# Kernel optimization log

Measured on AMD Instinct MI355X. Metric: run time of the kernel, lower is better.

The kernel has to match this reference:

```python
import jax, jax.numpy as jnp
import numpy as np

NEG = -1000000.0

def setup_inputs() -> dict:
    key = jax.random.key(0)
    ks = jax.random.split(key, 7)
    B, Lq, Lk, Dq, Dk, Dv, H = 4, 256, 1024, 512, 512, 512, 256
    return {
        "query": jax.random.normal(ks[0], (B, Lq, Dq), dtype=jnp.float32),
        "key": jax.random.normal(ks[1], (B, Lk, Dk), dtype=jnp.float32),
        "value": jax.random.normal(ks[2], (B, Lk, Dv), dtype=jnp.float32),
        "valid_len": jax.random.randint(ks[3], (B,), 1, Lk + 1),
        "Wq": jax.random.normal(ks[4], (Dq, H), dtype=jnp.float32) * (1.0 / np.sqrt(Dq)),
        "Wk": jax.random.normal(ks[5], (Dk, H), dtype=jnp.float32) * (1.0 / np.sqrt(Dk)),
        "wv": jax.random.normal(ks[6], (H,), dtype=jnp.float32) * (1.0 / np.sqrt(H)),
    }

def reference(query, key, value, valid_len, Wq, Wk, wv):
    # projections: [B,Lq,H], [B,Lk,H]
    q = jnp.einsum("bqd,dh->bqh", query, Wq)
    k = jnp.einsum("bkd,dh->bkh", key, Wk)
    # broadcast-add + tanh: [B,Lq,Lk,H]
    features = jnp.tanh(q[:, :, None, :] + k[:, None, :, :])
    # score projection to scalar: [B,Lq,Lk]
    score = jnp.einsum("bqkh,h->bqk", features, wv)
    # masked softmax over keys (valid_len per batch, broadcast over queries)
    Lk = key.shape[1]
    mask = jnp.arange(Lk)[None, None, :] < valid_len[:, None, None]
    score = jnp.where(mask, score, NEG)
    attn = jax.nn.softmax(score, axis=-1)
    # weighted sum of values: [B,Lq,Dv]  (dropout is identity in eval)
    return jnp.einsum("bqk,bkv->bqv", attn, value)
```

## Files before the change

### kernel.cpp

```cpp
#include <hip/hip_runtime.h>

typedef __attribute__((ext_vector_type(8))) short short8v;
typedef __attribute__((ext_vector_type(4))) float float4v;
typedef unsigned int uint;

#define TWO_LOG2E 2.8853900817779268f
#define LOG2E     1.4426950408889634f

__device__ inline uint rne_bf16(float x) {
    uint u = __float_as_uint(x);
    return (u + 0x7fffu + ((u >> 16) & 1u)) >> 16;
}
__device__ inline uint pack_hi_lo(float a0, float a1, uint& lo_pack) {
    const uint h0 = rne_bf16(a0), h1 = rne_bf16(a1);
    const float f0 = __uint_as_float(h0 << 16), f1 = __uint_as_float(h1 << 16);
    const float l0 = a0 - f0, l1 = a1 - f1;
    lo_pack = (rne_bf16(l1) << 16) | rne_bf16(l0);
    return (h1 << 16) | h0;
}

__global__ __launch_bounds__(256) void prep_a(
    const float* __restrict__ query, const float* __restrict__ key,
    const int* __restrict__ vlen,
    ushort* __restrict__ A_hi, ushort* __restrict__ A_lo)
{
    const int t = blockIdx.x * 256 + threadIdx.x;
    const int row = t >> 6;
    const int cg = (t & 63) * 8;
    if (row >= 1024) {
        const int kr = (row - 1024) & 1023, b = (row - 1024) >> 10;
        if ((kr & ~63) >= vlen[b]) return;
    }
    const float* src = (row < 1024) ? (query + (size_t)row * 512 + cg)
                                    : (key + (size_t)(row - 1024) * 512 + cg);
    const float4 x0 = *(const float4*)src;
    const float4 x1 = *(const float4*)(src + 4);
    uint h0, h1, h2, h3, l0, l1, l2, l3;
    h0 = pack_hi_lo(x0.x, x0.y, l0);
    h1 = pack_hi_lo(x0.z, x0.w, l1);
    h2 = pack_hi_lo(x1.x, x1.y, l2);
    h3 = pack_hi_lo(x1.z, x1.w, l3);
    *(uint4*)(A_hi + (size_t)row * 512 + cg) = make_uint4(h0, h1, h2, h3);
    *(uint4*)(A_lo + (size_t)row * 512 + cg) = make_uint4(l0, l1, l2, l3);
}

__global__ __launch_bounds__(256) void prep_w(
    const float* __restrict__ Wq, const float* __restrict__ Wk,
    ushort* __restrict__ WT_hi, ushort* __restrict__ WT_lo)
{
    const int t = blockIdx.x * 256 + threadIdx.x;
    const int n = t & 255;
    const int kg = ((t >> 8) & 63) * 8;
    const int w = t >> 14;
    const float* W = w ? Wk : Wq;
    float x[8];
    #pragma unroll
    for (int i = 0; i < 8; ++i) x[i] = W[(size_t)(kg + i) * 256 + n];
    uint h0, h1, h2, h3, l0, l1, l2, l3;
    h0 = pack_hi_lo(x[0], x[1], l0);
    h1 = pack_hi_lo(x[2], x[3], l1);
    h2 = pack_hi_lo(x[4], x[5], l2);
    h3 = pack_hi_lo(x[6], x[7], l3);
    const size_t off = ((size_t)w * 256 + n) * 512 + kg;
    *(uint4*)(WT_hi + off) = make_uint4(h0, h1, h2, h3);
    *(uint4*)(WT_lo + off) = make_uint4(l0, l1, l2, l3);
}

#define LOADF(s, kbase) { const int ko = (kbase) + half * 8;                              \
    _Pragma("unroll") for (int f = 0; f < 4; ++f) {                                       \
        ah##s[f] = *(const short8v*)(a_h + (size_t)(f * 16) * 512 + ko);                  \
        al##s[f] = *(const short8v*)(a_l + (size_t)(f * 16) * 512 + ko);                  \
        bh##s[f] = *(const short8v*)(wt_h + (size_t)(f * 16) * 512 + ko);                 \
        bl##s[f] = *(const short8v*)(wt_l + (size_t)(f * 16) * 512 + ko); } }

#define MFMAS(s)                                                                          \
    _Pragma("unroll") for (int mf = 0; mf < 4; ++mf)                                      \
    _Pragma("unroll") for (int nf = 0; nf < 4; ++nf) {                                    \
        acc[mf][nf] = __builtin_amdgcn_mfma_f32_16x16x32_bf16(ah##s[mf], bh##s[nf], acc[mf][nf], 0, 0, 0); \
        acc[mf][nf] = __builtin_amdgcn_mfma_f32_16x16x32_bf16(ah##s[mf], bl##s[nf], acc[mf][nf], 0, 0, 0); \
        acc[mf][nf] = __builtin_amdgcn_mfma_f32_16x16x32_bf16(al##s[mf], bh##s[nf], acc[mf][nf], 0, 0, 0); }

__global__ __launch_bounds__(64) void proj_mfma(
    const ushort* __restrict__ A_hi, const ushort* __restrict__ A_lo,
    const ushort* __restrict__ WT_hi, const ushort* __restrict__ WT_lo,
    const int* __restrict__ valid_len,
    float* __restrict__ EqT, float* __restrict__ EkT)
{
    const int lane = threadIdx.x;
    const int n0 = blockIdx.x * 64;
    const int m0 = blockIdx.y * 64;
    const bool isq = (m0 < 1024);
    int b = 0, kk0 = 0;
    if (!isq) {
        kk0 = (m0 - 1024) & 1023;
        b = (m0 - 1024) >> 10;
        if (kk0 >= valid_len[b]) return;
    }
    const int r = lane & 15, half = lane >> 4;
    const size_t wsel = isq ? 0 : (size_t)256 * 512;
    const ushort* wt_h = WT_hi + wsel + (size_t)(n0 + r) * 512;
    const ushort* wt_l = WT_lo + wsel + (size_t)(n0 + r) * 512;
    const ushort* a_h = A_hi + (size_t)(m0 + r) * 512;
    const ushort* a_l = A_lo + (size_t)(m0 + r) * 512;

    float4v acc[4][4] = {{{0.f}}};
    short8v ah0[4], al0[4], bh0[4], bl0[4];
    short8v ah1[4], al1[4], bh1[4], bl1[4];

    LOADF(0, 0);
    for (int kt = 0; kt < 512; kt += 64) {
        LOADF(1, kt + 32);
        MFMAS(0);
        if (kt + 64 < 512) LOADF(0, kt + 64);
        MFMAS(1);
    }

    #pragma unroll
    for (int mf = 0; mf < 4; ++mf) {
        #pragma unroll
        for (int nf = 0; nf < 4; ++nf) {
            float4v e;
            #pragma unroll
            for (int i = 0; i < 4; ++i)
                e[i] = __builtin_amdgcn_exp2f(acc[mf][nf][i] * TWO_LOG2E);
            if (isq) {
                *(float4v*)(EqT + (size_t)(n0 + nf * 16 + r) * 1024 +
                            m0 + mf * 16 + half * 4) = e;
            } else {
                *(float4v*)(EkT + (size_t)(b * 256 + n0 + nf * 16 + r) * 1024 +
                            kk0 + mf * 16 + half * 4) = e;
            }
        }
    }
}

__global__ __launch_bounds__(1024) void score_softmax_kernel(
    const float* __restrict__ EqT, const float* __restrict__ EkT,
    const float* __restrict__ wv, const int* __restrict__ valid_len,
    float* __restrict__ attn)
{
    __shared__ float wv_s[256];
    __shared__ float eq4_s[256 * 4];
    __shared__ float red[16][4];

    const int tid = threadIdx.x;
    const int b = blockIdx.x >> 6;
    const int q0 = (blockIdx.x & 63) << 2;

    const int vlen = valid_len[b];
    const int k = tid;
    const bool v = (k < vlen);

    if (tid < 256) {
        wv_s[tid] = wv[tid];
        *(float4*)&eq4_s[tid * 4] =
            *(const float4*)(EqT + (size_t)tid * 1024 + b * 256 + q0);
    }
    __syncthreads();

    float acc[4] = {};
    float cw = 0.f;

    if (v) {
        const float* ekp = EkT + (size_t)(b * 256) * 1024 + k;
        #pragma unroll 8
        for (int h = 0; h < 256; ++h) {
            const float ek = ekp[(size_t)h * 1024];
            const float4 eq = *(const float4*)&eq4_s[h * 4];
            const float w = wv_s[h];
            cw += w;
            acc[0] = fmaf(w, __builtin_amdgcn_rcpf(fmaf(eq.x, ek, 1.f)), acc[0]);
            acc[1] = fmaf(w, __builtin_amdgcn_rcpf(fmaf(eq.y, ek, 1.f)), acc[1]);
            acc[2] = fmaf(w, __builtin_amdgcn_rcpf(fmaf(eq.z, ek, 1.f)), acc[2]);
            acc[3] = fmaf(w, __builtin_amdgcn_rcpf(fmaf(eq.w, ek, 1.f)), acc[3]);
        }
    }

    float s[4], m[4];
    #pragma unroll
    for (int q = 0; q < 4; ++q) {
        s[q] = fmaf(-2.f, acc[q], cw);
        m[q] = v ? s[q] : -1e30f;
    }
    #pragma unroll
    for (int o = 32; o; o >>= 1) {
        #pragma unroll
        for (int q = 0; q < 4; ++q) m[q] = fmaxf(m[q], __shfl_xor(m[q], o));
    }
    const int wid = tid >> 6;
    if ((tid & 63) == 0) {
        #pragma unroll
        for (int q = 0; q < 4; ++q) red[wid][q] = m[q];
    }
    __syncthreads();
    #pragma unroll
    for (int q = 0; q < 4; ++q) {
        float mm = red[0][q];
        #pragma unroll
        for (int w = 1; w < 16; ++w) mm = fmaxf(mm, red[w][q]);
        m[q] = mm;
    }
    __syncthreads();

    float p[4], l[4];
    #pragma unroll
    for (int q = 0; q < 4; ++q) {
        p[q] = v ? __builtin_amdgcn_exp2f((s[q] - m[q]) * LOG2E) : 0.f;
        l[q] = p[q];
    }
    #pragma unroll
    for (int o = 32; o; o >>= 1) {
        #pragma unroll
        for (int q = 0; q < 4; ++q) l[q] += __shfl_xor(l[q], o);
    }
    if ((tid & 63) == 0) {
        #pragma unroll
        for (int q = 0; q < 4; ++q) red[wid][q] = l[q];
    }
    __syncthreads();
    #pragma unroll
    for (int q = 0; q < 4; ++q) {
        float ss = red[0][q];
        #pragma unroll
        for (int w = 1; w < 16; ++w) ss += red[w][q];
        const float rl = __builtin_amdgcn_rcpf(ss);
        attn[(size_t)(b * 256 + q0 + q) * 1024 + k] = p[q] * rl;
    }
}

__global__ __launch_bounds__(256) void pv_kernel(
    const float* __restrict__ attn, const float* __restrict__ value,
    const int* __restrict__ valid_len,
    float* __restrict__ out)
{
    __shared__ float As[32][34];
    __shared__ float Bs[32][64];

    const int tid = threadIdx.x;
    const int b = blockIdx.z;
    const int m0 = blockIdx.y * 32, n0 = blockIdx.x * 64;
    const float* A = attn + ((size_t)b * 256 + m0) * 1024;
    const float* B = value + (size_t)b * 1024 * 512;

    const int kend = (valid_len[b] + 31) & ~31;

    const int tx = tid & 15, ty = tid >> 4;
    const int lr = tid >> 3, lc = (tid & 7) * 4;
    const int br = tid >> 4, bc = (tid & 15) * 4;

    float4 av  = *(const float4*)(A + (size_t)lr * 1024 + lc);
    float4 bv0 = *(const float4*)(B + (size_t)br * 512 + n0 + bc);
    float4 bv1 = *(const float4*)(B + (size_t)(br + 16) * 512 + n0 + bc);

    float c[2][4] = {};

    for (int kt = 0; kt < kend; kt += 32) {
        __syncthreads();
        As[lc + 0][lr] = av.x; As[lc + 1][lr] = av.y;
        As[lc + 2][lr] = av.z; As[lc + 3][lr] = av.w;
        *(float4*)&Bs[br][bc] = bv0;
        *(float4*)&Bs[br + 16][bc] = bv1;
        __syncthreads();
        if (kt + 32 < kend) {
            av  = *(const float4*)(A + (size_t)lr * 1024 + kt + 32 + lc);
            bv0 = *(const float4*)(B + (size_t)(kt + 32 + br) * 512 + n0 + bc);
            bv1 = *(const float4*)(B + (size_t)(kt + 48 + br) * 512 + n0 + bc);
        }
        #pragma unroll
        for (int k = 0; k < 32; ++k) {
            const float2 a = *(const float2*)&As[k][ty * 2];
            const float4 bb = *(const float4*)&Bs[k][tx * 4];
            c[0][0] = fmaf(a.x, bb.x, c[0][0]);
            c[0][1] = fmaf(a.x, bb.y, c[0][1]);
            c[0][2] = fmaf(a.x, bb.z, c[0][2]);
            c[0][3] = fmaf(a.x, bb.w, c[0][3]);
            c[1][0] = fmaf(a.y, bb.x, c[1][0]);
            c[1][1] = fmaf(a.y, bb.y, c[1][1]);
            c[1][2] = fmaf(a.y, bb.z, c[1][2]);
            c[1][3] = fmaf(a.y, bb.w, c[1][3]);
        }
    }

    #pragma unroll
    for (int i = 0; i < 2; ++i) {
        float4 o;
        o.x = c[i][0]; o.y = c[i][1]; o.z = c[i][2]; o.w = c[i][3];
        *(float4*)(out + (size_t)b * 256 * 512 +
                   (size_t)(m0 + ty * 2 + i) * 512 + n0 + tx * 4) = o;
    }
}

extern "C" void kernel_launch(void* const* d_in, const int* in_sizes, int n_in,
                              void* d_out, int out_size, void* d_ws, size_t ws_size,
                              hipStream_t stream)
{
    const float* query = (const float*)d_in[0];
    const float* key   = (const float*)d_in[1];
    const float* value = (const float*)d_in[2];
    const int*   vlen  = (const int*)d_in[3];
    const float* Wq    = (const float*)d_in[4];
    const float* Wk    = (const float*)d_in[5];
    const float* wv    = (const float*)d_in[6];
    float* out = (float*)d_out;

    float*  EqT   = (float*)d_ws;
    float*  EkT   = EqT + 262144;
    float*  attn  = EkT + 1048576;
    ushort* A_hi  = (ushort*)(attn + 1048576);
    ushort* A_lo  = A_hi + 2621440;
    ushort* WT_hi = A_lo + 2621440;
    ushort* WT_lo = WT_hi + 262144;

    hipLaunchKernelGGL(prep_w, dim3(128), dim3(256), 0, stream,
                       Wq, Wk, WT_hi, WT_lo);
    hipLaunchKernelGGL(prep_a, dim3(1280), dim3(256), 0, stream,
                       query, key, vlen, A_hi, A_lo);
    hipLaunchKernelGGL(proj_mfma, dim3(4, 80), dim3(64), 0, stream,
                       A_hi, A_lo, WT_hi, WT_lo, vlen, EqT, EkT);
    hipLaunchKernelGGL(score_softmax_kernel, dim3(256), dim3(1024), 0, stream,
                       EqT, EkT, wv, vlen, attn);
    hipLaunchKernelGGL(pv_kernel, dim3(8, 8, 4), dim3(256), 0, stream,
                       attn, value, vlen, out);
}
```

Measured before the change: 84.06 us.

## Split score into H-halved partial kernel with 16-query tiles, separate softmax

The fused score+softmax kernel becomes a partial-score kernel and a separate softmax kernel. The partial kernel tiles 16 queries by 256 keys and splits the hidden dimension in two halves, writing partial sums that the softmax kernel adds. The projection GEMM tile is halved in M to launch more blocks. This is meant to raise parallelism and reuse of each loaded key value. It costs extra global traffic for the partial score buffers and an extra launch.

```diff
diff --git a/kernel.cpp b/kernel.cpp
--- a/kernel.cpp
+++ b/kernel.cpp
@@ -66,15 +66,16 @@
     *(uint4*)(WT_lo + off) = make_uint4(l0, l1, l2, l3);
 }
 
-#define LOADF(s, kbase) { const int ko = (kbase) + half * 8;                              \
-    _Pragma("unroll") for (int f = 0; f < 4; ++f) {                                       \
-        ah##s[f] = *(const short8v*)(a_h + (size_t)(f * 16) * 512 + ko);                  \
-        al##s[f] = *(const short8v*)(a_l + (size_t)(f * 16) * 512 + ko);                  \
-        bh##s[f] = *(const short8v*)(wt_h + (size_t)(f * 16) * 512 + ko);                 \
+#define LOADF(s, kbase) { const int ko = (kbase) + half * 8;                \
+    _Pragma("unroll") for (int f = 0; f < 2; ++f) {                         \
+        ah##s[f] = *(const short8v*)(a_h + (size_t)(f * 16) * 512 + ko);    \
+        al##s[f] = *(const short8v*)(a_l + (size_t)(f * 16) * 512 + ko); }  \
+    _Pragma("unroll") for (int f = 0; f < 4; ++f) {                         \
+        bh##s[f] = *(const short8v*)(wt_h + (size_t)(f * 16) * 512 + ko);   \
         bl##s[f] = *(const short8v*)(wt_l + (size_t)(f * 16) * 512 + ko); } }
 
 #define MFMAS(s)                                                                          \
-    _Pragma("unroll") for (int mf = 0; mf < 4; ++mf)                                      \
+    _Pragma("unroll") for (int mf = 0; mf < 2; ++mf)                                      \
     _Pragma("unroll") for (int nf = 0; nf < 4; ++nf) {                                    \
         acc[mf][nf] = __builtin_amdgcn_mfma_f32_16x16x32_bf16(ah##s[mf], bh##s[nf], acc[mf][nf], 0, 0, 0); \
         acc[mf][nf] = __builtin_amdgcn_mfma_f32_16x16x32_bf16(ah##s[mf], bl##s[nf], acc[mf][nf], 0, 0, 0); \
@@ -88,7 +89,7 @@
 {
     const int lane = threadIdx.x;
     const int n0 = blockIdx.x * 64;
-    const int m0 = blockIdx.y * 64;
+    const int m0 = blockIdx.y * 32;
     const bool isq = (m0 < 1024);
     int b = 0, kk0 = 0;
     if (!isq) {
@@ -103,9 +104,9 @@
     const ushort* a_h = A_hi + (size_t)(m0 + r) * 512;
     const ushort* a_l = A_lo + (size_t)(m0 + r) * 512;
 
-    float4v acc[4][4] = {{{0.f}}};
-    short8v ah0[4], al0[4], bh0[4], bl0[4];
-    short8v ah1[4], al1[4], bh1[4], bl1[4];
+    float4v acc[2][4] = {{{0.f}}};
+    short8v ah0[2], al0[2], bh0[4], bl0[4];
+    short8v ah1[2], al1[2], bh1[4], bl1[4];
 
     LOADF(0, 0);
     for (int kt = 0; kt < 512; kt += 64) {
@@ -116,7 +117,7 @@
     }
 
     #pragma unroll
-    for (int mf = 0; mf < 4; ++mf) {
+    for (int mf = 0; mf < 2; ++mf) {
         #pragma unroll
         for (int nf = 0; nf < 4; ++nf) {
             float4v e;
@@ -134,13 +135,68 @@
     }
 }
 
-__global__ __launch_bounds__(1024) void score_softmax_kernel(
+__global__ __launch_bounds__(256) void score_partial(
     const float* __restrict__ EqT, const float* __restrict__ EkT,
     const float* __restrict__ wv, const int* __restrict__ valid_len,
-    float* __restrict__ attn)
-{
-    __shared__ float wv_s[256];
-    __shared__ float eq4_s[256 * 4];
+    float* __restrict__ P0, float* __restrict__ P1)
+{
+    __shared__ float wv_s[128];
+    __shared__ float eqs[128][16];
+
+    const int orig = blockIdx.x;
+    const int wg = (orig & 7) * 64 + (orig >> 3);
+    const int qg = wg & 15;
+    const int kq = (wg >> 4) & 3;
+    const int hh = (wg >> 6) & 1;
+    const int b  = wg >> 7;
+
+    const int tid = threadIdx.x;
+    const int vlen = valid_len[b];
+    if (kq * 256 >= vlen) return;
+    const int k = kq * 256 + tid;
+    const int q0 = qg * 16;
+
+    if (tid < 128) {
+        wv_s[tid] = wv[hh * 128 + tid];
+        const float* ep = EqT + (size_t)(hh * 128 + tid) * 1024 + b * 256 + q0;
+        #pragma unroll
+        for (int j = 0; j < 4; ++j)
+            *(float4*)&eqs[tid][j * 4] = *(const float4*)(ep + j * 4);
+    }
+    __syncthreads();
+
+    float acc[16] = {};
+    float cw = 0.f;
+    const bool v = (k < vlen);
+
+    if (v) {
+        const float* ekp = EkT + ((size_t)(b * 256 + hh * 128)) * 1024 + k;
+        #pragma unroll 2
+        for (int h = 0; h < 128; ++h) {
+            const float ek = ekp[(size_t)h * 1024];
+            const float w = wv_s[h];
+            cw += w;
+            #pragma unroll
+            for (int j = 0; j < 4; ++j) {
+                const float4 eq = *(const float4*)&eqs[h][j * 4];
+                acc[j*4+0] = fmaf(w, __builtin_amdgcn_rcpf(fmaf(eq.x, ek, 1.f)), acc[j*4+0]);
+                acc[j*4+1] = fmaf(w, __builtin_amdgcn_rcpf(fmaf(eq.y, ek, 1.f)), acc[j*4+1]);
+                acc[j*4+2] = fmaf(w, __builtin_amdgcn_rcpf(fmaf(eq.z, ek, 1.f)), acc[j*4+2]);
+                acc[j*4+3] = fmaf(w, __builtin_amdgcn_rcpf(fmaf(eq.w, ek, 1.f)), acc[j*4+3]);
+            }
+        }
+    }
+
+    float* __restrict__ P = hh ? P1 : P0;
+    #pragma unroll
+    for (int qi = 0; qi < 16; ++qi)
+        P[(size_t)(b * 256 + q0 + qi) * 1024 + k] = fmaf(-2.f, acc[qi], cw);
+}
+
+__global__ __launch_bounds__(1024) void softmax_kernel(
+    const float* __restrict__ P1, const int* __restrict__ valid_len,
+    float* __restrict__ attn )
+{
     __shared__ float red[16][4];
 
     const int tid = threadIdx.x;
@@ -151,35 +207,11 @@
     const int k = tid;
     const bool v = (k < vlen);
 
-    if (tid < 256) {
-        wv_s[tid] = wv[tid];
-        *(float4*)&eq4_s[tid * 4] =
-            *(const float4*)(EqT + (size_t)tid * 1024 + b * 256 + q0);
-    }
-    __syncthreads();
-
-    float acc[4] = {};
-    float cw = 0.f;
-
-    if (v) {
-        const float* ekp = EkT + (size_t)(b * 256) * 1024 + k;
-        #pragma unroll 8
-        for (int h = 0; h < 256; ++h) {
-            const float ek = ekp[(size_t)h * 1024];
-            const float4 eq = *(const float4*)&eq4_s[h * 4];
-            const float w = wv_s[h];
-            cw += w;
-            acc[0] = fmaf(w, __builtin_amdgcn_rcpf(fmaf(eq.x, ek, 1.f)), acc[0]);
-            acc[1] = fmaf(w, __builtin_amdgcn_rcpf(fmaf(eq.y, ek, 1.f)), acc[1]);
-            acc[2] = fmaf(w, __builtin_amdgcn_rcpf(fmaf(eq.z, ek, 1.f)), acc[2]);
-            acc[3] = fmaf(w, __builtin_amdgcn_rcpf(fmaf(eq.w, ek, 1.f)), acc[3]);
-        }
-    }
-
     float s[4], m[4];
     #pragma unroll
     for (int q = 0; q < 4; ++q) {
-        s[q] = fmaf(-2.f, acc[q], cw);
+        const size_t off = (size_t)(b * 256 + q0 + q) * 1024 + k;
+        s[q] = attn[off] + P1[off];
         m[q] = v ? s[q] : -1e30f;
     }
     #pragma unroll
@@ -305,8 +337,9 @@
 
     float*  EqT   = (float*)d_ws;
     float*  EkT   = EqT + 262144;
-    float*  attn  = EkT + 1048576;
-    ushort* A_hi  = (ushort*)(attn + 1048576);
+    float*  P0    = EkT + 1048576;
+    float*  P1    = P0 + 1048576;
+    ushort* A_hi  = (ushort*)(P1 + 1048576);
     ushort* A_lo  = A_hi + 2621440;
     ushort* WT_hi = A_lo + 2621440;
     ushort* WT_lo = WT_hi + 262144;
@@ -315,10 +348,12 @@
                        Wq, Wk, WT_hi, WT_lo);
     hipLaunchKernelGGL(prep_a, dim3(1280), dim3(256), 0, stream,
                        query, key, vlen, A_hi, A_lo);
-    hipLaunchKernelGGL(proj_mfma, dim3(4, 80), dim3(64), 0, stream,
+    hipLaunchKernelGGL(proj_mfma, dim3(4, 160), dim3(64), 0, stream,
                        A_hi, A_lo, WT_hi, WT_lo, vlen, EqT, EkT);
-    hipLaunchKernelGGL(score_softmax_kernel, dim3(256), dim3(1024), 0, stream,
-                       EqT, EkT, wv, vlen, attn);
+    hipLaunchKernelGGL(score_partial, dim3(512), dim3(256), 0, stream,
+                       EqT, EkT, wv, vlen, P0, P1);
+    hipLaunchKernelGGL(softmax_kernel, dim3(256), dim3(1024), 0, stream,
+                       P1, vlen, P0);
     hipLaunchKernelGGL(pv_kernel, dim3(8, 8, 4), dim3(256), 0, stream,
-                       attn, value, vlen, out);
-}
+                       P0, value, vlen, out);
+}
```

Measured after the change: 97.40 us. +15.9%, slower.

## Move PV matmul to split-bf16 MFMA and retile projection and score kernels

Applied to the files above, without the earlier changes.

Replaces the fp32 FMA attention-times-value kernel with an MFMA kernel that uses a hi/lo bf16 split. A new prep_v kernel transposes and splits value, and the score kernel now writes attention as hi/lo bf16. The score kernel processes two keys per thread with 512 threads and drops the constant wv-sum term, since softmax is invariant to a per-row shift. The projection MFMA tile is halved in M to launch twice as many blocks. The cost is an extra transpose kernel and more workspace traffic, and precision depends on the three-product bf16 split.

```diff
diff --git a/kernel.cpp b/kernel.cpp
--- a/kernel.cpp
+++ b/kernel.cpp
@@ -66,15 +66,51 @@
     *(uint4*)(WT_lo + off) = make_uint4(l0, l1, l2, l3);
 }
 
-#define LOADF(s, kbase) { const int ko = (kbase) + half * 8;                              \
-    _Pragma("unroll") for (int f = 0; f < 4; ++f) {                                       \
-        ah##s[f] = *(const short8v*)(a_h + (size_t)(f * 16) * 512 + ko);                  \
-        al##s[f] = *(const short8v*)(a_l + (size_t)(f * 16) * 512 + ko);                  \
-        bh##s[f] = *(const short8v*)(wt_h + (size_t)(f * 16) * 512 + ko);                 \
+__global__ __launch_bounds__(256) void prep_v(
+    const float* __restrict__ value, const int* __restrict__ vlen,
+    ushort* __restrict__ VT_hi, ushort* __restrict__ VT_lo)
+{
+    __shared__ float t[64][69];
+    const int b = blockIdx.z;
+    const int k0 = blockIdx.y * 64, n0 = blockIdx.x * 64;
+    const int kendB = (vlen[b] + 31) & ~31;
+    if (k0 >= kendB) return;
+
+    const int tid = threadIdx.x;
+    const int n_in = (tid & 15) * 4, k_in = tid >> 4;
+    const float* src = value + ((size_t)b * 1024 + k0 + k_in) * 512 + n0 + n_in;
+    #pragma unroll
+    for (int p = 0; p < 4; ++p) {
+        const float4 x = *(const float4*)(src + (size_t)p * 16 * 512);
+        t[k_in + p * 16][n_in + 0] = x.x;
+        t[k_in + p * 16][n_in + 1] = x.y;
+        t[k_in + p * 16][n_in + 2] = x.z;
+        t[k_in + p * 16][n_in + 3] = x.w;
+    }
+    __syncthreads();
+
+    const int rn = tid >> 2, c0 = (tid & 3) * 16;
+    uint hp[8], lp[8];
+    #pragma unroll
+    for (int i = 0; i < 8; ++i)
+        hp[i] = pack_hi_lo(t[c0 + 2 * i][rn], t[c0 + 2 * i + 1][rn], lp[i]);
+    const size_t off = ((size_t)b * 512 + n0 + rn) * 1024 + k0 + c0;
+    *(uint4*)(VT_hi + off) = make_uint4(hp[0], hp[1], hp[2], hp[3]);
+    *(uint4*)(VT_hi + off + 8) = make_uint4(hp[4], hp[5], hp[6], hp[7]);
+    *(uint4*)(VT_lo + off) = make_uint4(lp[0], lp[1], lp[2], lp[3]);
+    *(uint4*)(VT_lo + off + 8) = make_uint4(lp[4], lp[5], lp[6], lp[7]);
+}
+
+#define LOADF(s, kbase) { const int ko = (kbase) + half * 8;                \
+    _Pragma("unroll") for (int f = 0; f < 2; ++f) {                         \
+        ah##s[f] = *(const short8v*)(a_h + (size_t)(f * 16) * 512 + ko);    \
+        al##s[f] = *(const short8v*)(a_l + (size_t)(f * 16) * 512 + ko); }  \
+    _Pragma("unroll") for (int f = 0; f < 4; ++f) {                         \
+        bh##s[f] = *(const short8v*)(wt_h + (size_t)(f * 16) * 512 + ko);   \
         bl##s[f] = *(const short8v*)(wt_l + (size_t)(f * 16) * 512 + ko); } }
 
 #define MFMAS(s)                                                                          \
-    _Pragma("unroll") for (int mf = 0; mf < 4; ++mf)                                      \
+    _Pragma("unroll") for (int mf = 0; mf < 2; ++mf)                                      \
     _Pragma("unroll") for (int nf = 0; nf < 4; ++nf) {                                    \
         acc[mf][nf] = __builtin_amdgcn_mfma_f32_16x16x32_bf16(ah##s[mf], bh##s[nf], acc[mf][nf], 0, 0, 0); \
         acc[mf][nf] = __builtin_amdgcn_mfma_f32_16x16x32_bf16(ah##s[mf], bl##s[nf], acc[mf][nf], 0, 0, 0); \
@@ -88,7 +124,7 @@
 {
     const int lane = threadIdx.x;
     const int n0 = blockIdx.x * 64;
-    const int m0 = blockIdx.y * 64;
+    const int m0 = blockIdx.y * 32;
     const bool isq = (m0 < 1024);
     int b = 0, kk0 = 0;
     if (!isq) {
@@ -103,9 +139,9 @@
     const ushort* a_h = A_hi + (size_t)(m0 + r) * 512;
     const ushort* a_l = A_lo + (size_t)(m0 + r) * 512;
 
-    float4v acc[4][4] = {{{0.f}}};
-    short8v ah0[4], al0[4], bh0[4], bl0[4];
-    short8v ah1[4], al1[4], bh1[4], bl1[4];
+    float4v acc[2][4] = {{{0.f}}};
+    short8v ah0[2], al0[2], bh0[4], bl0[4];
+    short8v ah1[2], al1[2], bh1[4], bl1[4];
 
     LOADF(0, 0);
     for (int kt = 0; kt < 512; kt += 64) {
@@ -116,7 +152,7 @@
     }
 
     #pragma unroll
-    for (int mf = 0; mf < 4; ++mf) {
+    for (int mf = 0; mf < 2; ++mf) {
         #pragma unroll
         for (int nf = 0; nf < 4; ++nf) {
             float4v e;
@@ -134,22 +170,22 @@
     }
 }
 
-__global__ __launch_bounds__(1024) void score_softmax_kernel(
+__global__ __launch_bounds__(512) void score_softmax_kernel(
     const float* __restrict__ EqT, const float* __restrict__ EkT,
     const float* __restrict__ wv, const int* __restrict__ valid_len,
-    float* __restrict__ attn)
+    ushort* __restrict__ attn_hi, ushort* __restrict__ attn_lo)
 {
     __shared__ float wv_s[256];
     __shared__ float eq4_s[256 * 4];
-    __shared__ float red[16][4];
+    __shared__ float red[8][4];
 
     const int tid = threadIdx.x;
     const int b = blockIdx.x >> 6;
     const int q0 = (blockIdx.x & 63) << 2;
 
     const int vlen = valid_len[b];
-    const int k = tid;
-    const bool v = (k < vlen);
+    const int k0 = tid * 2;
+    const bool v0 = (k0 < vlen), v1 = (k0 + 1 < vlen);
 
     if (tid < 256) {
         wv_s[tid] = wv[tid];
@@ -158,29 +194,35 @@
     }
     __syncthreads();
 
-    float acc[4] = {};
-    float cw = 0.f;
-
-    if (v) {
-        const float* ekp = EkT + (size_t)(b * 256) * 1024 + k;
-        #pragma unroll 8
+    float acc[4][2] = {};
+
+    if (v0) {
+        const float* ekp = EkT + (size_t)(b * 256) * 1024 + k0;
+        #pragma unroll 4
         for (int h = 0; h < 256; ++h) {
-            const float ek = ekp[(size_t)h * 1024];
+            const float2 ek = *(const float2*)(ekp + (size_t)h * 1024);
             const float4 eq = *(const float4*)&eq4_s[h * 4];
             const float w = wv_s[h];
-            cw += w;
-            acc[0] = fmaf(w, __builtin_amdgcn_rcpf(fmaf(eq.x, ek, 1.f)), acc[0]);
-            acc[1] = fmaf(w, __builtin_amdgcn_rcpf(fmaf(eq.y, ek, 1.f)), acc[1]);
-            acc[2] = fmaf(w, __builtin_amdgcn_rcpf(fmaf(eq.z, ek, 1.f)), acc[2]);
-            acc[3] = fmaf(w, __builtin_amdgcn_rcpf(fmaf(eq.w, ek, 1.f)), acc[3]);
+            acc[0][0] = fmaf(w, __builtin_amdgcn_rcpf(fmaf(eq.x, ek.x, 1.f)), acc[0][0]);
+            acc[0][1] = fmaf(w, __builtin_amdgcn_rcpf(fmaf(eq.x, ek.y, 1.f)), acc[0][1]);
+            acc[1][0] = fmaf(w, __builtin_amdgcn_rcpf(fmaf(eq.y, ek.x, 1.f)), acc[1][0]);
+            acc[1][1] = fmaf(w, __builtin_amdgcn_rcpf(fmaf(eq.y, ek.y, 1.f)), acc[1][1]);
+            acc[2][0] = fmaf(w, __builtin_amdgcn_rcpf(fmaf(eq.z, ek.x, 1.f)), acc[2][0]);
+            acc[2][1] = fmaf(w, __builtin_amdgcn_rcpf(fmaf(eq.z, ek.y, 1.f)), acc[2][1]);
+            acc[3][0] = fmaf(w, __builtin_amdgcn_rcpf(fmaf(eq.w, ek.x, 1.f)), acc[3][0]);
+            acc[3][1] = fmaf(w, __builtin_amdgcn_rcpf(fmaf(eq.w, ek.y, 1.f)), acc[3][1]);
         }
     }
 
-    float s[4], m[4];
+    float s[4][2], m[4];
     #pragma unroll
     for (int q = 0; q < 4; ++q) {
-        s[q] = fmaf(-2.f, acc[q], cw);
-        m[q] = v ? s[q] : -1e30f;
+        s[q][0] = -2.f * acc[q][0];
+        s[q][1] = -2.f * acc[q][1];
+        float mm = -1e30f;
+        if (v0) mm = s[q][0];
+        if (v1) mm = fmaxf(mm, s[q][1]);
+        m[q] = mm;
     }
     #pragma unroll
     for (int o = 32; o; o >>= 1) {
@@ -197,16 +239,17 @@
     for (int q = 0; q < 4; ++q) {
         float mm = red[0][q];
         #pragma unroll
-        for (int w = 1; w < 16; ++w) mm = fmaxf(mm, red[w][q]);
+        for (int w = 1; w < 8; ++w) mm = fmaxf(mm, red[w][q]);
         m[q] = mm;
     }
     __syncthreads();
 
-    float p[4], l[4];
+    float p[4][2], l[4];
     #pragma unroll
     for (int q = 0; q < 4; ++q) {
-        p[q] = v ? __builtin_amdgcn_exp2f((s[q] - m[q]) * LOG2E) : 0.f;
-        l[q] = p[q];
+        p[q][0] = v0 ? __builtin_amdgcn_exp2f((s[q][0] - m[q]) * LOG2E) : 0.f;
+        p[q][1] = v1 ? __builtin_amdgcn_exp2f((s[q][1] - m[q]) * LOG2E) : 0.f;
+        l[q] = p[q][0] + p[q][1];
     }
     #pragma unroll
     for (int o = 32; o; o >>= 1) {
@@ -222,71 +265,68 @@
     for (int q = 0; q < 4; ++q) {
         float ss = red[0][q];
         #pragma unroll
-        for (int w = 1; w < 16; ++w) ss += red[w][q];
+        for (int w = 1; w < 8; ++w) ss += red[w][q];
         const float rl = __builtin_amdgcn_rcpf(ss);
-        attn[(size_t)(b * 256 + q0 + q) * 1024 + k] = p[q] * rl;
-    }
-}
-
-__global__ __launch_bounds__(256) void pv_kernel(
-    const float* __restrict__ attn, const float* __restrict__ value,
+        const float a0 = p[q][0] * rl, a1 = p[q][1] * rl;
+        uint lo;
+        const uint hi = pack_hi_lo(a0, a1, lo);
+        const size_t off = (size_t)(b * 256 + q0 + q) * 1024 + k0;
+        *(uint*)(attn_hi + off) = hi;
+        *(uint*)(attn_lo + off) = lo;
+    }
+}
+
+#define PVLOAD(s, ko) {                                   \
+    ah##s = *(const short8v*)(ah_p + (ko));               \
+    al##s = *(const short8v*)(al_p + (ko));               \
+    bh0##s = *(const short8v*)(bh_p + (ko));              \
+    bl0##s = *(const short8v*)(bl_p + (ko));              \
+    bh1##s = *(const short8v*)(bh_p + 16 * 1024 + (ko));  \
+    bl1##s = *(const short8v*)(bl_p + 16 * 1024 + (ko)); }
+
+#define PVMFMA(s) {                                                              \
+    acc0 = __builtin_amdgcn_mfma_f32_16x16x32_bf16(ah##s, bh0##s, acc0, 0, 0, 0); \
+    acc0 = __builtin_amdgcn_mfma_f32_16x16x32_bf16(ah##s, bl0##s, acc0, 0, 0, 0); \
+    acc0 = __builtin_amdgcn_mfma_f32_16x16x32_bf16(al##s, bh0##s, acc0, 0, 0, 0); \
+    acc1 = __builtin_amdgcn_mfma_f32_16x16x32_bf16(ah##s, bh1##s, acc1, 0, 0, 0); \
+    acc1 = __builtin_amdgcn_mfma_f32_16x16x32_bf16(ah##s, bl1##s, acc1, 0, 0, 0); \
+    acc1 = __builtin_amdgcn_mfma_f32_16x16x32_bf16(al##s, bh1##s, acc1, 0, 0, 0); }
+
+__global__ __launch_bounds__(64) void pv_mfma(
+    const ushort* __restrict__ attn_hi, const ushort* __restrict__ attn_lo,
+    const ushort* __restrict__ VT_hi, const ushort* __restrict__ VT_lo,
     const int* __restrict__ valid_len,
     float* __restrict__ out)
 {
-    __shared__ float As[32][34];
-    __shared__ float Bs[32][64];
-
-    const int tid = threadIdx.x;
+    const int lane = threadIdx.x;
+    const int n0 = blockIdx.x * 32;
+    const int q0 = blockIdx.y * 16;
     const int b = blockIdx.z;
-    const int m0 = blockIdx.y * 32, n0 = blockIdx.x * 64;
-    const float* A = attn + ((size_t)b * 256 + m0) * 1024;
-    const float* B = value + (size_t)b * 1024 * 512;
-
+    const int r = lane & 15, half = lane >> 4;
     const int kend = (valid_len[b] + 31) & ~31;
 
-    const int tx = tid & 15, ty = tid >> 4;
-    const int lr = tid >> 3, lc = (tid & 7) * 4;
-    const int br = tid >> 4, bc = (tid & 15) * 4;
-
-    float4 av  = *(const float4*)(A + (size_t)lr * 1024 + lc);
-    float4 bv0 = *(const float4*)(B + (size_t)br * 512 + n0 + bc);
-    float4 bv1 = *(const float4*)(B + (size_t)(br + 16) * 512 + n0 + bc);
-
-    float c[2][4] = {};
-
-    for (int kt = 0; kt < kend; kt += 32) {
-        __syncthreads();
-        As[lc + 0][lr] = av.x; As[lc + 1][lr] = av.y;
-        As[lc + 2][lr] = av.z; As[lc + 3][lr] = av.w;
-        *(float4*)&Bs[br][bc] = bv0;
-        *(float4*)&Bs[br + 16][bc] = bv1;
-        __syncthreads();
-        if (kt + 32 < kend) {
-            av  = *(const float4*)(A + (size_t)lr * 1024 + kt + 32 + lc);
-            bv0 = *(const float4*)(B + (size_t)(kt + 32 + br) * 512 + n0 + bc);
-            bv1 = *(const float4*)(B + (size_t)(kt + 48 + br) * 512 + n0 + bc);
-        }
-        #pragma unroll
-        for (int k = 0; k < 32; ++k) {
-            const float2 a = *(const float2*)&As[k][ty * 2];
-            const float4 bb = *(const float4*)&Bs[k][tx * 4];
-            c[0][0] = fmaf(a.x, bb.x, c[0][0]);
-            c[0][1] = fmaf(a.x, bb.y, c[0][1]);
-            c[0][2] = fmaf(a.x, bb.z, c[0][2]);
-            c[0][3] = fmaf(a.x, bb.w, c[0][3]);
-            c[1][0] = fmaf(a.y, bb.x, c[1][0]);
-            c[1][1] = fmaf(a.y, bb.y, c[1][1]);
-            c[1][2] = fmaf(a.y, bb.z, c[1][2]);
-            c[1][3] = fmaf(a.y, bb.w, c[1][3]);
-        }
-    }
-
-    #pragma unroll
-    for (int i = 0; i < 2; ++i) {
-        float4 o;
-        o.x = c[i][0]; o.y = c[i][1]; o.z = c[i][2]; o.w = c[i][3];
-        *(float4*)(out + (size_t)b * 256 * 512 +
-                   (size_t)(m0 + ty * 2 + i) * 512 + n0 + tx * 4) = o;
+    const ushort* ah_p = attn_hi + (size_t)(b * 256 + q0 + r) * 1024 + half * 8;
+    const ushort* al_p = attn_lo + (size_t)(b * 256 + q0 + r) * 1024 + half * 8;
+    const ushort* bh_p = VT_hi + (size_t)(b * 512 + n0 + r) * 1024 + half * 8;
+    const ushort* bl_p = VT_lo + (size_t)(b * 512 + n0 + r) * 1024 + half * 8;
+
+    float4v acc0 = {0.f}, acc1 = {0.f};
+    short8v ah0, al0, bh00, bl00, bh10, bl10;
+    short8v ah1, al1, bh01, bl01, bh11, bl11;
+
+    PVLOAD(0, 0);
+    for (int kt = 0; kt < kend; kt += 64) {
+        if (kt + 32 < kend) PVLOAD(1, kt + 32);
+        PVMFMA(0);
+        if (kt + 64 < kend) PVLOAD(0, kt + 64);
+        if (kt + 32 < kend) PVMFMA(1);
+    }
+
+    float* op = out + (size_t)b * 256 * 512 + (size_t)(q0 + half * 4) * 512 + n0 + r;
+    #pragma unroll
+    for (int i = 0; i < 4; ++i) {
+        op[(size_t)i * 512] = acc0[i];
+        op[(size_t)i * 512 + 16] = acc1[i];
     }
 }
 
@@ -303,22 +343,27 @@
     const float* wv    = (const float*)d_in[6];
     float* out = (float*)d_out;
 
-    float*  EqT   = (float*)d_ws;
-    float*  EkT   = EqT + 262144;
-    float*  attn  = EkT + 1048576;
-    ushort* A_hi  = (ushort*)(attn + 1048576);
-    ushort* A_lo  = A_hi + 2621440;
-    ushort* WT_hi = A_lo + 2621440;
-    ushort* WT_lo = WT_hi + 262144;
+    float*  EqT     = (float*)d_ws;
+    float*  EkT     = EqT + 262144;
+    ushort* A_hi    = (ushort*)(EkT + 1048576);
+    ushort* A_lo    = A_hi + 2621440;
+    ushort* WT_hi   = A_lo + 2621440;
+    ushort* WT_lo   = WT_hi + 262144;
+    ushort* attn_hi = WT_lo + 262144;
+    ushort* attn_lo = attn_hi + 1048576;
+    ushort* VT_hi   = attn_lo + 1048576;
+    ushort* VT_lo   = VT_hi + 2097152;
 
     hipLaunchKernelGGL(prep_w, dim3(128), dim3(256), 0, stream,
                        Wq, Wk, WT_hi, WT_lo);
     hipLaunchKernelGGL(prep_a, dim3(1280), dim3(256), 0, stream,
                        query, key, vlen, A_hi, A_lo);
-    hipLaunchKernelGGL(proj_mfma, dim3(4, 80), dim3(64), 0, stream,
+    hipLaunchKernelGGL(prep_v, dim3(8, 16, 4), dim3(256), 0, stream,
+                       value, vlen, VT_hi, VT_lo);
+    hipLaunchKernelGGL(proj_mfma, dim3(4, 160), dim3(64), 0, stream,
                        A_hi, A_lo, WT_hi, WT_lo, vlen, EqT, EkT);
-    hipLaunchKernelGGL(score_softmax_kernel, dim3(256), dim3(1024), 0, stream,
-                       EqT, EkT, wv, vlen, attn);
-    hipLaunchKernelGGL(pv_kernel, dim3(8, 8, 4), dim3(256), 0, stream,
-                       attn, value, vlen, out);
-}
+    hipLaunchKernelGGL(score_softmax_kernel, dim3(256), dim3(512), 0, stream,
+                       EqT, EkT, wv, vlen, attn_hi, attn_lo);
+    hipLaunchKernelGGL(pv_mfma, dim3(16, 16, 4), dim3(64), 0, stream,
+                       attn_hi, attn_lo, VT_hi, VT_lo, vlen, out);
+}
```

After: 87.03 us. +3.5%, slower.
